# Kernel optimization log

Hardware: AMD Instinct MI355X
Metric: run time of the kernel (lower is better)

Reference implementation:

```python
import jax, jax.numpy as jnp
import numpy as np

N_VIEWS, N_JOINTS, HM_H, HM_W = 5, 15, 128, 240
P = 4
VX = VY = VZ = 64
FX = FY = 253
FZ = 64
WHOLE_SIZE = np.array([8000.0, 8000.0, 2000.0], np.float32)
CENTER = np.array([0.0, -500.0, 800.0], np.float32)
IND_SIZE = np.array([2000.0, 2000.0, 2000.0], np.float32)
FINE = np.array([FX, FY, FZ], np.float32)


def setup_inputs() -> dict:
    key = jax.random.key(0)
    k1, k2, k3, k4 = jax.random.split(key, 4)
    heatmaps = jax.random.uniform(k1, (N_VIEWS, N_JOINTS, HM_H, HM_W), jnp.float32)
    # cached per-view fine-voxel sampling grid, clamped to [-1.1, 1.1] as in project_grid
    sample_grids = jax.random.uniform(k2, (N_VIEWS, FX, FY, FZ, 2), jnp.float32) * 2.2 - 1.1
    xyz = jnp.asarray(CENTER) + (jax.random.uniform(k3, (P, 3), jnp.float32) - 0.5) * jnp.asarray(WHOLE_SIZE - IND_SIZE)
    wh = jax.random.uniform(k4, (P, 2), jnp.float32, minval=0.2, maxval=1.0)
    proposal_centers = jnp.concatenate([xyz, jnp.zeros((P, 2), jnp.float32), wh], axis=1)
    return {"heatmaps": heatmaps, "sample_grids": sample_grids, "proposal_centers": proposal_centers}


def _grid_sample_2d(img, gx, gy):
    # img: [J,H,W]; gx,gy: [...]  bilinear, align_corners=True, zero padding (torch defaults)
    H, W = img.shape[-2:]
    px = (gx + 1.0) * 0.5 * (W - 1)
    py = (gy + 1.0) * 0.5 * (H - 1)
    x0 = jnp.floor(px)
    y0 = jnp.floor(py)
    wx1 = px - x0
    wy1 = py - y0

    def pick(xi, yi):
        ok = ((xi >= 0) & (xi < W) & (yi >= 0) & (yi < H)).astype(img.dtype)
        xc = jnp.clip(xi, 0, W - 1).astype(jnp.int32)
        yc = jnp.clip(yi, 0, H - 1).astype(jnp.int32)
        return img[:, yc, xc] * ok  # [J, ...]

    return (pick(x0, y0) * ((1 - wx1) * (1 - wy1))
            + pick(x0 + 1, y0) * (wx1 * (1 - wy1))
            + pick(x0, y0 + 1) * ((1 - wx1) * wy1)
            + pick(x0 + 1, y0 + 1) * (wx1 * wy1))


def _grids():
    # self.grids: computed once from INDIVIDUAL space size around whole-space center
    gx = np.linspace(-IND_SIZE[0] / 2, IND_SIZE[0] / 2, VX) + CENTER[0]
    gy = np.linspace(-IND_SIZE[1] / 2, IND_SIZE[1] / 2, VY) + CENTER[1]
    gz = np.linspace(-IND_SIZE[2] / 2, IND_SIZE[2] / 2, VZ) + CENTER[2]
    grid = np.stack(np.meshgrid(gx, gy, gz, indexing='ij'), axis=-1)  # [VX,VY,VZ,3]
    grids = np.stack([grid[:, :, 0, :2].reshape(-1, 2),
                      grid[:, 0, :, ::2].reshape(-1, 2),
                      grid[0, :, :, 1:].reshape(-1, 2)])
    return jnp.asarray(grids, jnp.float32)


def _forward(heatmaps, sample_grids, proposal_centers):
    pc = jax.lax.stop_gradient(proposal_centers)  # index math is non-differentiable
    mask_x = jnp.maximum(((1.0 - pc[:, 5]) / 2.0 * (VX - 1)).astype(jnp.int32), 0)
    mask_y = jnp.maximum(((1.0 - pc[:, 6]) / 2.0 * (VY - 1)).astype(jnp.int32), 0)
    ctl = jnp.round((pc[:, 0:3] + jnp.asarray(WHOLE_SIZE) / 2.0 - jnp.asarray(CENTER)
                     - jnp.asarray(IND_SIZE) / 2.0) / jnp.asarray(WHOLE_SIZE)
                    * (jnp.asarray(FINE) - 1.0)).astype(jnp.int32)
    x, y, z = ctl[:, 0], ctl[:, 1], ctl[:, 2]
    x_start = jnp.maximum(-x, 0) + mask_x
    x_end = jnp.minimum(FX - x, VX) - mask_x
    y_start = jnp.maximum(-y, 0) + mask_y
    y_end = jnp.minimum(FY - y, VY) - mask_y
    z_start = jnp.maximum(-z, 0)
    z_end = jnp.minimum(FZ - z, VZ)

    ix = jnp.arange(VX)
    iy = jnp.arange(VY)
    iz = jnp.arange(VZ)
    vx = (ix[None, :] >= x_start[:, None]) & (ix[None, :] < x_end[:, None])  # [P,VX]
    vy = (iy[None, :] >= y_start[:, None]) & (iy[None, :] < y_end[:, None])
    vz = (iz[None, :] >= z_start[:, None]) & (iz[None, :] < z_end[:, None])
    valid = vx[:, :, None, None] & vy[:, None, :, None] & vz[:, None, None, :]  # [P,VX,VY,VZ]

    # fine-grid indices for every output voxel (clipped; invalid ones masked out)
    fx = jnp.clip(x[:, None] + ix[None, :], 0, FX - 1)  # [P,VX]
    fy = jnp.clip(y[:, None] + iy[None, :], 0, FY - 1)
    fz = jnp.clip(z[:, None] + iz[None, :], 0, FZ - 1)
    sg = sample_grids[:, fx[:, :, None, None], fy[:, None, :, None], fz[:, None, None, :], :]  # [n,P,VX,VY,VZ,2]

    sampled = jax.vmap(_grid_sample_2d)(heatmaps, sg[..., 0], sg[..., 1])  # [n,J,P,VX,VY,VZ]
    cubes = jnp.mean(sampled, axis=0).transpose(1, 0, 2, 3, 4)  # [P,J,VX,VY,VZ]
    cubes = jnp.clip(cubes * valid[:, None, :, :, :].astype(cubes.dtype), 0.0, 1.0)
    return cubes


def reference(heatmaps, sample_grids, proposal_centers):
    cubes = _forward(heatmaps, sample_grids, proposal_centers)
    return (cubes, _grids())
```

## Files before the change

kernel.cpp:

```cpp
#include <hip/hip_runtime.h>

#define N_VIEWS 5
#define N_JOINTS 15
#define HM_H 128
#define HM_W 240
#define PB 4
#define VXn 64
#define VYn 64
#define VZn 64
#define FXn 253
#define FYn 253
#define FZn 64
#define JP 16

typedef float        vf2 __attribute__((ext_vector_type(2)));
typedef unsigned int vu4 __attribute__((ext_vector_type(4)));

#define T_TOTAL (N_VIEWS * HM_H * HM_W)
#define G_TOTAL (3 * 4096)

__global__ void prep_kernel(const float* __restrict__ hm,
                            unsigned char* __restrict__ T,
                            float* __restrict__ gout) {
    int t = blockIdx.x * blockDim.x + threadIdx.x;
    if (t < T_TOTAL) {
        int x = t % HM_W;
        int vy = t / HM_W;
        int y = vy % HM_H;
        int v = vy / HM_H;
        unsigned int w[4] = {0u, 0u, 0u, 0u};
#pragma unroll
        for (int j = 0; j < N_JOINTS; ++j) {
            float val = hm[(((size_t)v * N_JOINTS + j) * HM_H + y) * HM_W + x];
            float q = rintf(val * 255.0f);
            q = fminf(fmaxf(q, 0.0f), 255.0f);
            w[j >> 2] |= ((unsigned int)q) << ((j & 3) * 8);
        }
        vu4* dst = (vu4*)(T + (size_t)t * JP);
        vu4 o; o.x = w[0]; o.y = w[1]; o.z = w[2]; o.w = w[3];
        *dst = o;
    } else {
        int u = t - T_TOTAL;
        if (u >= G_TOTAL) return;
        int g = u / 4096;
        int idx = u % 4096;
        int a = idx / 64;
        int b = idx % 64;
        const float step = 2000.0f / 63.0f;
        float va = -1000.0f + (float)a * step;
        float vb = -1000.0f + (float)b * step;
        float o0, o1;
        if (g == 0)      { o0 = va + 0.0f;      o1 = vb + (-500.0f); }
        else if (g == 1) { o0 = va + 0.0f;      o1 = vb + 800.0f;    }
        else             { o0 = va + (-500.0f); o1 = vb + 800.0f;    }
        gout[(size_t)u * 2 + 0] = o0;
        gout[(size_t)u * 2 + 1] = o1;
    }
}

__global__ __launch_bounds__(256, 3) void project_kernel(
    const unsigned char* __restrict__ hmT,
    const float* __restrict__ sg,
    const float* __restrict__ pc,
    float* __restrict__ out)
{
    const int iz = threadIdx.x;
    const int iy = blockIdx.x * 4 + threadIdx.y;
    const int ix = blockIdx.y;
    const int p  = blockIdx.z;

    const float pw = pc[p * 7 + 5];
    const float ph = pc[p * 7 + 6];
    int mask_x = max((int)((1.0f - pw) / 2.0f * (float)(VXn - 1)), 0);
    int mask_y = max((int)((1.0f - ph) / 2.0f * (float)(VYn - 1)), 0);

    float tx = pc[p * 7 + 0] + 4000.0f; tx = tx - 0.0f;      tx = tx - 1000.0f;
    float ty = pc[p * 7 + 1] + 4000.0f; ty = ty - (-500.0f); ty = ty - 1000.0f;
    float tz = pc[p * 7 + 2] + 1000.0f; tz = tz - 800.0f;    tz = tz - 1000.0f;
    tx = tx / 8000.0f * 252.0f;
    ty = ty / 8000.0f * 252.0f;
    tz = tz / 2000.0f * 63.0f;
    int cx = (int)rintf(tx);
    int cy = (int)rintf(ty);
    int cz = (int)rintf(tz);

    int x_start = max(-cx, 0) + mask_x;
    int x_end   = min(FXn - cx, VXn) - mask_x;
    int y_start = max(-cy, 0) + mask_y;
    int y_end   = min(FYn - cy, VYn) - mask_y;
    int z_start = max(-cz, 0);
    int z_end   = min(FZn - cz, VZn);

    const bool valid = (ix >= x_start && ix < x_end) &&
                       (iy >= y_start && iy < y_end) &&
                       (iz >= z_start && iz < z_end);

    const size_t out_base = ((((size_t)p * N_JOINTS) * VXn + ix) * VYn + iy) * VZn + iz;
    const size_t out_jstride = (size_t)VXn * VYn * VZn;

    unsigned long long mv = __ballot(valid ? 1 : 0);
    if (mv == 0ull) {
#pragma unroll
        for (int j = 0; j < N_JOINTS; ++j)
            __builtin_nontemporal_store(0.0f, &out[out_base + j * out_jstride]);
        return;
    }

    const int fx = min(max(cx + ix, 0), FXn - 1);
    const int fy = min(max(cy + iy, 0), FYn - 1);
    const int fz = min(max(cz + iz, 0), FZn - 1);

    const size_t sg_base = (((size_t)fx * FYn + fy) * FZn + fz) * 2;
    const size_t sg_vstride = (size_t)FXn * FYn * FZn * 2;

    vf2 g[N_VIEWS];
#pragma unroll
    for (int v = 0; v < N_VIEWS; ++v)
        g[v] = __builtin_nontemporal_load(
            (const vf2*)(sg + sg_base + (size_t)v * sg_vstride));

    float w00[N_VIEWS], w10[N_VIEWS], w01[N_VIEWS], w11[N_VIEWS];
    unsigned off00[N_VIEWS], off10[N_VIEWS], off01[N_VIEWS], off11[N_VIEWS];
#pragma unroll
    for (int v = 0; v < N_VIEWS; ++v) {
        float px = (g[v].x + 1.0f) * 0.5f * (float)(HM_W - 1);
        float py = (g[v].y + 1.0f) * 0.5f * (float)(HM_H - 1);
        float x0f = floorf(px), y0f = floorf(py);
        float wx1 = px - x0f,  wy1 = py - y0f;
        float wx0 = 1.0f - wx1, wy0 = 1.0f - wy1;
        float x1f = x0f + 1.0f, y1f = y0f + 1.0f;
        float okx0 = (x0f >= 0.0f && x0f < (float)HM_W) ? 1.0f : 0.0f;
        float okx1 = (x1f >= 0.0f && x1f < (float)HM_W) ? 1.0f : 0.0f;
        float oky0 = (y0f >= 0.0f && y0f < (float)HM_H) ? 1.0f : 0.0f;
        float oky1 = (y1f >= 0.0f && y1f < (float)HM_H) ? 1.0f : 0.0f;
        int x0 = min(max((int)x0f, 0), HM_W - 1);
        int x1 = min(max((int)x0f + 1, 0), HM_W - 1);
        int y0 = min(max((int)y0f, 0), HM_H - 1);
        int y1 = min(max((int)y0f + 1, 0), HM_H - 1);
        w00[v] = wx0 * wy0 * okx0 * oky0;
        w10[v] = wx1 * wy0 * okx1 * oky0;
        w01[v] = wx0 * wy1 * okx0 * oky1;
        w11[v] = wx1 * wy1 * okx1 * oky1;
        unsigned vbase = (unsigned)(v * HM_H * HM_W);
        off00[v] = (vbase + (unsigned)y0 * HM_W + (unsigned)x0) * JP;
        off10[v] = (vbase + (unsigned)y0 * HM_W + (unsigned)x1) * JP;
        off01[v] = (vbase + (unsigned)y1 * HM_W + (unsigned)x0) * JP;
        off11[v] = (vbase + (unsigned)y1 * HM_W + (unsigned)x1) * JP;
    }

    vu4 tap[N_VIEWS][4];
#pragma unroll
    for (int v = 0; v < N_VIEWS; ++v) {
        tap[v][0] = *(const vu4*)(hmT + off00[v]);
        tap[v][1] = *(const vu4*)(hmT + off10[v]);
        tap[v][2] = *(const vu4*)(hmT + off01[v]);
        tap[v][3] = *(const vu4*)(hmT + off11[v]);
    }

    float acc[N_JOINTS];
#pragma unroll
    for (int j = 0; j < N_JOINTS; ++j) acc[j] = 0.0f;

#pragma unroll
    for (int v = 0; v < N_VIEWS; ++v) {
        const unsigned int* a = (const unsigned int*)&tap[v][0];
        const unsigned int* b = (const unsigned int*)&tap[v][1];
        const unsigned int* c = (const unsigned int*)&tap[v][2];
        const unsigned int* d = (const unsigned int*)&tap[v][3];
#pragma unroll
        for (int j = 0; j < N_JOINTS; ++j) {
            int word = j >> 2, sh = (j & 3) * 8;
            float fa = (float)((a[word] >> sh) & 0xffu);
            float fb = (float)((b[word] >> sh) & 0xffu);
            float fc = (float)((c[word] >> sh) & 0xffu);
            float fd = (float)((d[word] >> sh) & 0xffu);
            acc[j] += w00[v] * fa + w10[v] * fb + w01[v] * fc + w11[v] * fd;
        }
    }

    const float scale = valid ? (0.2f / 255.0f) : 0.0f;
#pragma unroll
    for (int j = 0; j < N_JOINTS; ++j) {
        float vlu = acc[j] * scale;
        vlu = fminf(fmaxf(vlu, 0.0f), 1.0f);
        __builtin_nontemporal_store(vlu, &out[out_base + j * out_jstride]);
    }
}

extern "C" void kernel_launch(void* const* d_in, const int* in_sizes, int n_in,
                              void* d_out, int out_size, void* d_ws, size_t ws_size,
                              hipStream_t stream) {
    const float* hm = (const float*)d_in[0];
    const float* sg = (const float*)d_in[1];
    const float* pc = (const float*)d_in[2];
    float* out = (float*)d_out;

    unsigned char* T = (unsigned char*)d_ws;

    const size_t grids_off = (size_t)PB * N_JOINTS * VXn * VYn * VZn;
    const int prep_total = T_TOTAL + G_TOTAL;
    prep_kernel<<<(prep_total + 255) / 256, 256, 0, stream>>>(hm, T, out + grids_off);

    dim3 blk(64, 4, 1);
    dim3 grd(16, 64, 4);
    project_kernel<<<grd, blk, 0, stream>>>(T, sg, pc, out);
}
```

Before: 66.06 us.

## Use buffer loads for tap gathers, smaller blocks, plain output stores

Replaces the global-pointer gathers from the quantized heatmap table with raw buffer loads through a buffer resource descriptor, passing a cache-policy flag and leaving the compiler's fallback path if the builtin is missing. Block size drops from 256 to 128 threads with twice as many blocks, and the launch-bounds occupancy hint is removed. The nontemporal output stores become ordinary stores. The changes aim to cut address arithmetic and adjust scheduling and caching, but they mix several independent effects and the output stores may now pollute the cache.

```diff
diff --git a/kernel.cpp b/kernel.cpp
--- a/kernel.cpp
+++ b/kernel.cpp
@@ -15,9 +15,17 @@
 
 typedef float        vf2 __attribute__((ext_vector_type(2)));
 typedef unsigned int vu4 __attribute__((ext_vector_type(4)));
+typedef int          vi4 __attribute__((ext_vector_type(4)));
 
 #define T_TOTAL (N_VIEWS * HM_H * HM_W)
 #define G_TOTAL (3 * 4096)
+#define TABLE_BYTES (T_TOTAL * JP)
+
+#if defined(__has_builtin)
+#if __has_builtin(__builtin_amdgcn_make_buffer_rsrc) && __has_builtin(__builtin_amdgcn_raw_ptr_buffer_load_b128)
+#define USE_BUFLOAD 1
+#endif
+#endif
 
 __global__ void prep_kernel(const float* __restrict__ hm,
                             unsigned char* __restrict__ T,
@@ -58,14 +66,14 @@
     }
 }
 
-__global__ __launch_bounds__(256, 3) void project_kernel(
+__global__ __launch_bounds__(128) void project_kernel(
     const unsigned char* __restrict__ hmT,
     const float* __restrict__ sg,
     const float* __restrict__ pc,
     float* __restrict__ out)
 {
-    const int iz = threadIdx.x;
-    const int iy = blockIdx.x * 4 + threadIdx.y;
+    const int iz = threadIdx.x & 63;
+    const int iy = blockIdx.x * 2 + (threadIdx.x >> 6);
     const int ix = blockIdx.y;
     const int p  = blockIdx.z;
 
@@ -102,7 +110,7 @@
     if (mv == 0ull) {
 #pragma unroll
         for (int j = 0; j < N_JOINTS; ++j)
-            __builtin_nontemporal_store(0.0f, &out[out_base + j * out_jstride]);
+            out[out_base + j * out_jstride] = 0.0f;
         return;
     }
 
@@ -148,6 +156,18 @@
         off11[v] = (vbase + (unsigned)y1 * HM_W + (unsigned)x1) * JP;
     }
 
+#if USE_BUFLOAD
+    __amdgpu_buffer_rsrc_t rs = __builtin_amdgcn_make_buffer_rsrc(
+        (void*)hmT, (short)0, (int)TABLE_BYTES, 0x00020000);
+    vi4 tap[N_VIEWS][4];
+#pragma unroll
+    for (int v = 0; v < N_VIEWS; ++v) {
+        tap[v][0] = __builtin_amdgcn_raw_ptr_buffer_load_b128(rs, (int)off00[v], 0, 1);
+        tap[v][1] = __builtin_amdgcn_raw_ptr_buffer_load_b128(rs, (int)off10[v], 0, 1);
+        tap[v][2] = __builtin_amdgcn_raw_ptr_buffer_load_b128(rs, (int)off01[v], 0, 1);
+        tap[v][3] = __builtin_amdgcn_raw_ptr_buffer_load_b128(rs, (int)off11[v], 0, 1);
+    }
+#else
     vu4 tap[N_VIEWS][4];
 #pragma unroll
     for (int v = 0; v < N_VIEWS; ++v) {
@@ -156,6 +176,7 @@
         tap[v][2] = *(const vu4*)(hmT + off01[v]);
         tap[v][3] = *(const vu4*)(hmT + off11[v]);
     }
+#endif
 
     float acc[N_JOINTS];
 #pragma unroll
@@ -183,7 +204,7 @@
     for (int j = 0; j < N_JOINTS; ++j) {
         float vlu = acc[j] * scale;
         vlu = fminf(fmaxf(vlu, 0.0f), 1.0f);
-        __builtin_nontemporal_store(vlu, &out[out_base + j * out_jstride]);
+        out[out_base + j * out_jstride] = vlu;
     }
 }
 
@@ -201,7 +222,7 @@
     const int prep_total = T_TOTAL + G_TOTAL;
     prep_kernel<<<(prep_total + 255) / 256, 256, 0, stream>>>(hm, T, out + grids_off);
 
-    dim3 blk(64, 4, 1);
-    dim3 grd(16, 64, 4);
+    dim3 blk(128, 1, 1);
+    dim3 grd(32, 64, 4);
     project_kernel<<<grd, blk, 0, stream>>>(T, sg, pc, out);
 }
```

New measurement: 81.95 us. 1.24x slower.
